# Kernel optimization log

Measured on AMD Instinct MI355X. Metric: run time of the kernel, lower is better.

The kernel has to match this reference:

```python
import jax, jax.numpy as jnp
import numpy as np

B, N = 16384, 1024


def _bit_reversal_indices(n):
    bits = int(np.log2(n))
    val = np.arange(n)
    src = np.zeros(n, dtype=np.int64)
    for _ in range(bits):
        src = (src << 1) | (val & 1)
        val = val >> 1
    return src  # src[k] = source pair for target pair k


def _inter_stage_indices(n, stage_idx):
    prev = 2 ** stage_idx
    kb = np.arange(n // 2)
    g = kb // prev
    kw = kb % prev
    half = (kw >= prev // 2).astype(np.int64)
    off = kw % (prev // 2)
    nb = prev // 2
    sE = (2 * g) * nb + off
    sO = (2 * g + 1) * nb + off
    perm = np.empty(n, dtype=np.int64)
    perm[2 * kb] = 2 * sE + half
    perm[2 * kb + 1] = 2 * sO + half
    return perm


def _final_unscramble_indices(n):
    k = np.arange(n // 2)
    perm = np.empty(n, dtype=np.int64)
    perm[k] = 2 * k
    perm[k + n // 2] = 2 * k + 1
    return perm


def _butterfly_weights(n, stage_idx):
    # grouped 1x1 conv weights -> (n//2, 4, 4): out = W[g] @ in per group
    Nb = 2 ** (stage_idx + 1)
    nub = Nb // 2
    reps = n // Nb
    k = np.arange(nub)
    rW = np.cos(2.0 * np.pi * k / Nb)      # Re(W_Nb^k)
    iW = -np.sin(2.0 * np.pi * k / Nb)     # Im(W_Nb^k) (forward DFT twiddle)
    W = np.zeros((nub, 4, 4), dtype=np.float32)
    W[:, 0, 0] = 1.0; W[:, 0, 2] = rW;  W[:, 0, 3] = -iW
    W[:, 1, 1] = 1.0; W[:, 1, 2] = iW;  W[:, 1, 3] = rW
    W[:, 2, 0] = 1.0; W[:, 2, 2] = -rW; W[:, 2, 3] = iW
    W[:, 3, 1] = 1.0; W[:, 3, 2] = -iW; W[:, 3, 3] = -rW
    return np.tile(W, (reps, 1, 1))  # (n//2, 4, 4)


def setup_inputs() -> dict:
    key = jax.random.key(0)
    x = jax.random.normal(key, (B, 2 * N, 1, 1), dtype=jnp.float32)
    return {"x": x}


def reference(x) -> jnp.ndarray:
    b = x.shape[0]
    n = x.shape[1] // 2
    stages = int(np.log2(n))
    # pairs view: (B, N, 2) = interleaved [Re, Im]
    v = x.reshape(b, n, 2)
    v = v[:, jnp.asarray(_bit_reversal_indices(n)), :]
    for s in range(stages):
        if s > 0:
            v = v[:, jnp.asarray(_inter_stage_indices(n, s)), :]
        W = jnp.asarray(_butterfly_weights(n, s))       # (N/2, 4, 4)
        g = v.reshape(b, n // 2, 4)                     # 4 channels per group
        g = jnp.einsum('goi,bgi->bgo', W, g)            # grouped 1x1 conv
        v = g.reshape(b, n, 2)
    v = v[:, jnp.asarray(_final_unscramble_indices(n)), :]
    return v.reshape(b, 2 * n, 1, 1)
```

## Files before the change

### kernel.cpp

```cpp
#include <hip/hip_runtime.h>

#define NFFT 1024
#define TPB 256
#define RPW 2

__device__ __forceinline__ float2 cmul(float2 a, float2 b) {
  return make_float2(fmaf(a.x, b.x, -a.y * b.y), fmaf(a.x, b.y, a.y * b.x));
}
__device__ __forceinline__ float2 cadd(float2 a, float2 b) { return make_float2(a.x + b.x, a.y + b.y); }
__device__ __forceinline__ float2 csub(float2 a, float2 b) { return make_float2(a.x - b.x, a.y - b.y); }

__device__ __forceinline__ void dft4(const float2 v[4], float2 y[4]) {
  float2 s02 = cadd(v[0], v[2]), d02 = csub(v[0], v[2]);
  float2 s13 = cadd(v[1], v[3]), d13 = csub(v[1], v[3]);
  y[0] = cadd(s02, s13);
  y[2] = csub(s02, s13);
  y[1] = make_float2(d02.x + d13.y, d02.y - d13.x);
  y[3] = make_float2(d02.x - d13.y, d02.y + d13.x);
}

__device__ __forceinline__ float dpp_xor2(float x) {
  return __int_as_float(__builtin_amdgcn_update_dpp(0, __float_as_int(x), 0x4E, 0xF, 0xF, true));
}
__device__ __forceinline__ float dpp_xor1(float x) {
  return __int_as_float(__builtin_amdgcn_update_dpp(0, __float_as_int(x), 0xB1, 0xF, 0xF, true));
}

__device__ __forceinline__ void fft16(float2 z[16]) {
  float2 g[16];
  #pragma unroll
  for (int c0 = 0; c0 < 4; ++c0) {
    float2 v[4] = {z[c0], z[c0 + 4], z[c0 + 8], z[c0 + 12]};
    float2 y[4];
    dft4(v, y);
    g[4 * c0 + 0] = y[0]; g[4 * c0 + 1] = y[1]; g[4 * c0 + 2] = y[2]; g[4 * c0 + 3] = y[3];
  }
  const float C1 = 0.92387953251128674f, S1 = 0.38268343236508978f, R = 0.70710678118654752f;
  g[5]  = cmul(g[5],  make_float2( C1, -S1));
  g[6]  = cmul(g[6],  make_float2(  R,  -R));
  g[7]  = cmul(g[7],  make_float2( S1, -C1));
  g[9]  = cmul(g[9],  make_float2(  R,  -R));
  g[10] = make_float2(g[10].y, -g[10].x);
  g[11] = cmul(g[11], make_float2( -R,  -R));
  g[13] = cmul(g[13], make_float2( S1, -C1));
  g[14] = cmul(g[14], make_float2( -R,  -R));
  g[15] = cmul(g[15], make_float2(-C1,  S1));
  #pragma unroll
  for (int k0 = 0; k0 < 4; ++k0) {
    float2 v[4] = {g[k0], g[4 + k0], g[8 + k0], g[12 + k0]};
    float2 y[4];
    dft4(v, y);
    z[4 * k0 + 0] = y[0]; z[4 * k0 + 1] = y[1]; z[4 * k0 + 2] = y[2]; z[4 * k0 + 3] = y[3];
  }
}

__device__ __forceinline__ void twiddle_apply(float2 z[16], float2 u) {
  const float2 u2 = cmul(u, u);
  const float2 u4 = cmul(u2, u2);
  float2 c1 = u, c2 = u2, c3 = cmul(u2, u), c4 = u4;
  z[4]  = cmul(z[4],  c1); z[8]  = cmul(z[8],  c2);
  z[12] = cmul(z[12], c3); z[1]  = cmul(z[1],  c4);
  c1 = cmul(c1, u4); c2 = cmul(c2, u4); c3 = cmul(c3, u4); c4 = cmul(c4, u4);
  z[5]  = cmul(z[5],  c1); z[9]  = cmul(z[9],  c2);
  z[13] = cmul(z[13], c3); z[2]  = cmul(z[2],  c4);
  c1 = cmul(c1, u4); c2 = cmul(c2, u4); c3 = cmul(c3, u4); c4 = cmul(c4, u4);
  z[6]  = cmul(z[6],  c1); z[10] = cmul(z[10], c2);
  z[14] = cmul(z[14], c3); z[3]  = cmul(z[3],  c4);
  c1 = cmul(c1, u4); c2 = cmul(c2, u4); c3 = cmul(c3, u4);
  z[7]  = cmul(z[7],  c1); z[11] = cmul(z[11], c2); z[15] = cmul(z[15], c3);
}

__device__ __forceinline__ void procrow(float2 z[16], float2* __restrict__ buf,
                                        float2 u1, float2 u2, int lane,
                                        float2* __restrict__ dst) {
  fft16(z);
  twiddle_apply(z, u1);

  const int m = lane >> 2, p = lane & 3;
  #pragma unroll
  for (int s = 0; s < 16; ++s) {
    const int kap = (s >> 2) | ((s & 3) << 2);
    buf[m * 64 + ((p + 4 * kap) ^ ((m & 3) << 2))] = z[s];
  }
  asm volatile("s_waitcnt lgkmcnt(0)" ::: "memory");
  __builtin_amdgcn_sched_barrier(0);
  #pragma unroll
  for (int mm = 0; mm < 16; ++mm) z[mm] = buf[mm * 64 + (lane ^ ((mm & 3) << 2))];
  asm volatile("s_waitcnt lgkmcnt(0)" ::: "memory");
  __builtin_amdgcn_sched_barrier(0);

  fft16(z);
  twiddle_apply(z, u2);

  const float sgn1 = (lane & 2) ? -1.0f : 1.0f;
  const float sgn2 = (lane & 1) ? -1.0f : 1.0f;
  const bool tw3 = ((lane & 3) == 3);
  #pragma unroll
  for (int s = 0; s < 16; ++s) {
    float px = dpp_xor2(z[s].x), py = dpp_xor2(z[s].y);
    float ax = fmaf(sgn1, z[s].x, px), ay = fmaf(sgn1, z[s].y, py);
    float bx = tw3 ? ay : ax;
    float by = tw3 ? -ax : ay;
    float qx = dpp_xor1(bx), qy = dpp_xor1(by);
    z[s].x = fmaf(sgn2, bx, qx);
    z[s].y = fmaf(sgn2, by, qy);
  }

  const int kap = lane >> 2;
  const int ur = ((p & 1) << 1) | (p >> 1);
  float2* __restrict__ orow = dst + kap + 256 * ur;
  #pragma unroll
  for (int s = 0; s < 16; ++s) {
    const int t = (s >> 2) | ((s & 3) << 2);
    orow[16 * t] = z[s];
  }
}

__global__ __launch_bounds__(TPB, 4) void fft1024_kernel(const float* __restrict__ in,
                                                         float* __restrict__ out,
                                                         int nrows) {
  __shared__ __align__(16) float2 lds[TPB / 64][NFFT];
  const int wv = threadIdx.x >> 6;
  const int lane = threadIdx.x & 63;
  const int r0 = (blockIdx.x * (TPB / 64) + wv) * RPW;
  if (r0 >= nrows) return;

  const float2* __restrict__ xin = reinterpret_cast<const float2*>(in) + (size_t)r0 * NFFT;
  float2* __restrict__ xout = reinterpret_cast<float2*>(out) + (size_t)r0 * NFFT;
  float2* buf = lds[wv];

  float sn, cs;
  __sincosf((float)lane * (-6.2831853071795864769f / 1024.0f), &sn, &cs);
  const float2 u1 = make_float2(cs, sn);
  __sincosf((float)(lane & 3) * (-6.2831853071795864769f / 64.0f), &sn, &cs);
  const float2 u2 = make_float2(cs, sn);

  float2 A[16], B[16];
  #pragma unroll
  for (int c = 0; c < 16; ++c) A[c] = xin[lane + 64 * c];
  #pragma unroll
  for (int c = 0; c < 16; ++c) B[c] = xin[NFFT + lane + 64 * c];
  procrow(A, buf, u1, u2, lane, xout);
  procrow(B, buf, u1, u2, lane, xout + NFFT);
}

extern "C" void kernel_launch(void* const* d_in, const int* in_sizes, int n_in,
                              void* d_out, int out_size, void* d_ws, size_t ws_size,
                              hipStream_t stream) {
  const float* x = (const float*)d_in[0];
  float* out = (float*)d_out;
  const int rows = in_sizes[0] / (2 * NFFT);
  const int rpb = (TPB / 64) * RPW;
  const int blocks = (rows + rpb - 1) / rpb;
  fft1024_kernel<<<blocks, TPB, 0, stream>>>(x, out, rows);
}
```

Before: 241.1 us.

## Double-buffer rows via async global-to-LDS loads with 8 rows per wave

Each wave now processes 8 rows in a loop and prefetches the next row straight into a second LDS buffer with global_load_lds, so the load overlaps the current row's FFT. Row data is read from LDS instead of being held in registers, and launch bounds drop to 2 blocks per CU because LDS per block doubles. The hand-set vmcnt waits must match the number of outstanding loads and stores. Fewer blocks and lower occupancy could limit how well latency is hidden.

```diff
diff --git a/kernel.cpp b/kernel.cpp
--- a/kernel.cpp
+++ b/kernel.cpp
@@ -2,7 +2,10 @@
 
 #define NFFT 1024
 #define TPB 256
-#define RPW 2
+#define RPW 8
+
+typedef const __attribute__((address_space(1))) unsigned int gu32;
+typedef __attribute__((address_space(3))) unsigned int lu32;
 
 __device__ __forceinline__ float2 cmul(float2 a, float2 b) {
   return make_float2(fmaf(a.x, b.x, -a.y * b.y), fmaf(a.x, b.y, a.y * b.x));
@@ -70,64 +73,27 @@
   z[7]  = cmul(z[7],  c1); z[11] = cmul(z[11], c2); z[15] = cmul(z[15], c3);
 }
 
-__device__ __forceinline__ void procrow(float2 z[16], float2* __restrict__ buf,
-                                        float2 u1, float2 u2, int lane,
-                                        float2* __restrict__ dst) {
-  fft16(z);
-  twiddle_apply(z, u1);
-
-  const int m = lane >> 2, p = lane & 3;
+__device__ __forceinline__ void pref_row(const float4* __restrict__ g, float2* l, int lane) {
   #pragma unroll
-  for (int s = 0; s < 16; ++s) {
-    const int kap = (s >> 2) | ((s & 3) << 2);
-    buf[m * 64 + ((p + 4 * kap) ^ ((m & 3) << 2))] = z[s];
-  }
-  asm volatile("s_waitcnt lgkmcnt(0)" ::: "memory");
-  __builtin_amdgcn_sched_barrier(0);
-  #pragma unroll
-  for (int mm = 0; mm < 16; ++mm) z[mm] = buf[mm * 64 + (lane ^ ((mm & 3) << 2))];
-  asm volatile("s_waitcnt lgkmcnt(0)" ::: "memory");
-  __builtin_amdgcn_sched_barrier(0);
-
-  fft16(z);
-  twiddle_apply(z, u2);
-
-  const float sgn1 = (lane & 2) ? -1.0f : 1.0f;
-  const float sgn2 = (lane & 1) ? -1.0f : 1.0f;
-  const bool tw3 = ((lane & 3) == 3);
-  #pragma unroll
-  for (int s = 0; s < 16; ++s) {
-    float px = dpp_xor2(z[s].x), py = dpp_xor2(z[s].y);
-    float ax = fmaf(sgn1, z[s].x, px), ay = fmaf(sgn1, z[s].y, py);
-    float bx = tw3 ? ay : ax;
-    float by = tw3 ? -ax : ay;
-    float qx = dpp_xor1(bx), qy = dpp_xor1(by);
-    z[s].x = fmaf(sgn2, bx, qx);
-    z[s].y = fmaf(sgn2, by, qy);
-  }
-
-  const int kap = lane >> 2;
-  const int ur = ((p & 1) << 1) | (p >> 1);
-  float2* __restrict__ orow = dst + kap + 256 * ur;
-  #pragma unroll
-  for (int s = 0; s < 16; ++s) {
-    const int t = (s >> 2) | ((s & 3) << 2);
-    orow[16 * t] = z[s];
-  }
+  for (int j = 0; j < 8; ++j)
+    __builtin_amdgcn_global_load_lds((gu32*)(g + 64 * j + lane),
+                                     (lu32*)(l + 128 * j), 16, 0, 0);
 }
 
-__global__ __launch_bounds__(TPB, 4) void fft1024_kernel(const float* __restrict__ in,
+__global__ __launch_bounds__(TPB, 2) void fft1024_kernel(const float* __restrict__ in,
                                                          float* __restrict__ out,
                                                          int nrows) {
-  __shared__ __align__(16) float2 lds[TPB / 64][NFFT];
+  __shared__ __align__(16) float2 lds[TPB / 64][2][NFFT];
   const int wv = threadIdx.x >> 6;
   const int lane = threadIdx.x & 63;
-  const int r0 = (blockIdx.x * (TPB / 64) + wv) * RPW;
+  const long long w = (long long)blockIdx.x * (TPB / 64) + wv;
+  const long long r0 = w * RPW;
   if (r0 >= nrows) return;
 
-  const float2* __restrict__ xin = reinterpret_cast<const float2*>(in) + (size_t)r0 * NFFT;
-  float2* __restrict__ xout = reinterpret_cast<float2*>(out) + (size_t)r0 * NFFT;
-  float2* buf = lds[wv];
+  const float4* __restrict__ src = reinterpret_cast<const float4*>(in) + r0 * (NFFT / 2);
+  float2* __restrict__ dst = reinterpret_cast<float2*>(out) + r0 * NFFT;
+  float2* cur = lds[wv][0];
+  float2* nxt = lds[wv][1];
 
   float sn, cs;
   __sincosf((float)lane * (-6.2831853071795864769f / 1024.0f), &sn, &cs);
@@ -135,13 +101,66 @@
   __sincosf((float)(lane & 3) * (-6.2831853071795864769f / 64.0f), &sn, &cs);
   const float2 u2 = make_float2(cs, sn);
 
-  float2 A[16], B[16];
-  #pragma unroll
-  for (int c = 0; c < 16; ++c) A[c] = xin[lane + 64 * c];
-  #pragma unroll
-  for (int c = 0; c < 16; ++c) B[c] = xin[NFFT + lane + 64 * c];
-  procrow(A, buf, u1, u2, lane, xout);
-  procrow(B, buf, u1, u2, lane, xout + NFFT);
+  const int m = lane >> 2, p = lane & 3;
+  const float sgn1 = (lane & 2) ? -1.0f : 1.0f;
+  const float sgn2 = (lane & 1) ? -1.0f : 1.0f;
+  const bool tw3 = (p == 3);
+  const int kap = lane >> 2;
+  const int ur = ((p & 1) << 1) | (p >> 1);
+
+  pref_row(src, cur, lane);
+
+  #pragma unroll 1
+  for (int r = 0; r < RPW; ++r) {
+    if (r + 1 < RPW) pref_row(src + (long long)(r + 1) * (NFFT / 2), nxt, lane);
+
+    if (r == 0)            { asm volatile("s_waitcnt vmcnt(8)" ::: "memory"); }
+    else if (r + 1 < RPW)  { asm volatile("s_waitcnt vmcnt(24)" ::: "memory"); }
+    else                   { asm volatile("s_waitcnt vmcnt(16)" ::: "memory"); }
+    __builtin_amdgcn_sched_barrier(0);
+
+    float2 z[16];
+    #pragma unroll
+    for (int c = 0; c < 16; ++c) z[c] = cur[lane + 64 * c];
+
+    fft16(z);
+    twiddle_apply(z, u1);
+
+    #pragma unroll
+    for (int s = 0; s < 16; ++s) {
+      const int kp = (s >> 2) | ((s & 3) << 2);
+      cur[m * 64 + ((p + 4 * kp) ^ ((m & 3) << 2))] = z[s];
+    }
+    asm volatile("s_waitcnt lgkmcnt(0)" ::: "memory");
+    __builtin_amdgcn_sched_barrier(0);
+    #pragma unroll
+    for (int mm = 0; mm < 16; ++mm) z[mm] = cur[mm * 64 + (lane ^ ((mm & 3) << 2))];
+    asm volatile("s_waitcnt lgkmcnt(0)" ::: "memory");
+    __builtin_amdgcn_sched_barrier(0);
+
+    fft16(z);
+    twiddle_apply(z, u2);
+
+    #pragma unroll
+    for (int s = 0; s < 16; ++s) {
+      float px = dpp_xor2(z[s].x), py = dpp_xor2(z[s].y);
+      float ax = fmaf(sgn1, z[s].x, px), ay = fmaf(sgn1, z[s].y, py);
+      float bx = tw3 ? ay : ax;
+      float by = tw3 ? -ax : ay;
+      float qx = dpp_xor1(bx), qy = dpp_xor1(by);
+      z[s].x = fmaf(sgn2, bx, qx);
+      z[s].y = fmaf(sgn2, by, qy);
+    }
+
+    float2* __restrict__ orow = dst + (long long)r * NFFT + kap + 256 * ur;
+    #pragma unroll
+    for (int s = 0; s < 16; ++s) {
+      const int t = (s >> 2) | ((s & 3) << 2);
+      orow[16 * t] = z[s];
+    }
+
+    float2* tmp = cur; cur = nxt; nxt = tmp;
+  }
 }
 
 extern "C" void kernel_launch(void* const* d_in, const int* in_sizes, int n_in,
```

New measurement: 243.1 us. Within noise of the previous version (+0.8%).
